# Kernel tuning notes

Hardware: AMD Instinct MI355X
Metric: run time of the kernel (lower is better)

The kernel has to match this reference:

```python
import jax, jax.numpy as jnp
import numpy as np

PATCH = 3
COMPLETENESS = 2.0


def setup_inputs() -> dict:
    key = jax.random.key(0)
    k1, k2, k3 = jax.random.split(key, 3)
    C, Hs, Ws, Hr, Wr = 64, 512, 512, 512, 512
    ref = jax.random.normal(k1, (C, Hr, Wr), dtype=jnp.float32)
    nnf_sr = jax.random.randint(k2, (Hs, Ws, 2), 0, 512, dtype=jnp.int32)  # (ry, rx) per src pixel
    nnf_rs = jax.random.randint(k3, (Hr, Wr, 2), 0, 512, dtype=jnp.int32)  # (sy, sx) per ref pixel
    return {"ref": ref, "nnf_sr": nnf_sr, "nnf_rs": nnf_rs}


def bds_vote(ref, nnf_sr, nnf_rs, patch=PATCH, completeness=COMPLETENESS):
    C, Hr, Wr = ref.shape
    Hs, Ws = nnf_sr.shape[0], nnf_sr.shape[1]
    h = patch // 2
    ws = 1.0 / (Hs * Ws)
    wr = completeness / (Hr * Wr)

    guide = jnp.zeros((C, Hs * Ws), dtype=ref.dtype)
    weight = jnp.zeros((Hs * Ws,), dtype=ref.dtype)

    def accumulate(guide, weight, sy, sx, ry, rx, w):
        # sy,sx: target (src) centers [N]; ry,rx: source (ref) centers [N]
        # Clipped patch extents of the original code are equivalent to per-pixel
        # validity: both target and ref offset coords must be in range.
        for dy in range(-h, h + 1):
            for dx in range(-h, h + 1):
                ty, tx = sy + dy, sx + dx
                qy, qx = ry + dy, rx + dx
                valid = ((ty >= 0) & (ty < Hs) & (tx >= 0) & (tx < Ws) &
                         (qy >= 0) & (qy < Hr) & (qx >= 0) & (qx < Wr))
                vmask = valid.astype(ref.dtype) * w
                idx = jnp.clip(ty, 0, Hs - 1) * Ws + jnp.clip(tx, 0, Ws - 1)
                vals = ref[:, jnp.clip(qy, 0, Hr - 1), jnp.clip(qx, 0, Wr - 1)] * vmask[None, :]
                guide = guide.at[:, idx].add(vals)
                weight = weight.at[idx].add(vmask)
        return guide, weight

    # source -> reference pass (weight ws)
    gy, gx = jnp.meshgrid(jnp.arange(Hs), jnp.arange(Ws), indexing='ij')
    guide, weight = accumulate(guide, weight,
                               gy.reshape(-1), gx.reshape(-1),
                               nnf_sr[..., 0].reshape(-1), nnf_sr[..., 1].reshape(-1), ws)
    # reference -> source pass (weight wr)
    ry, rx = jnp.meshgrid(jnp.arange(Hr), jnp.arange(Wr), indexing='ij')
    guide, weight = accumulate(guide, weight,
                               nnf_rs[..., 0].reshape(-1), nnf_rs[..., 1].reshape(-1),
                               ry.reshape(-1), rx.reshape(-1), wr)

    weight = jnp.where(weight == 0, jnp.asarray(1.0, ref.dtype), weight)
    return (guide / weight[None, :]).reshape(C, Hs, Ws)


def reference(ref, nnf_sr, nnf_rs):
    return bds_vote(ref, nnf_sr, nnf_rs)
```

## Files before the change

### kernel.cpp

```cpp
#include <hip/hip_runtime.h>

#define HS   512
#define WSZ  512
#define NC   64
#define HW   (HS * WSZ)
#define KCAP 16

typedef unsigned int uint;
typedef unsigned short ushort;

__device__ __forceinline__ ushort f2bf(float f) {
    uint b = __float_as_uint(f);
    return (ushort)((b + 0x7FFFu + ((b >> 16) & 1u)) >> 16);
}

__global__ __launch_bounds__(256) void prep_kernel(
    const float4* __restrict__ ref4, uint4* __restrict__ refu4,
    int* __restrict__ cnt)
{
    __shared__ float lds[64 * 65];
    const int p0  = blockIdx.x * 64;
    const int tid = threadIdx.x;
    if (tid < 64) cnt[blockIdx.x * 64 + tid] = 0;
#pragma unroll
    for (int k = 0; k < 4; ++k) {
        int e  = k * 256 + tid;
        int c  = e >> 4;
        int i4 = e & 15;
        float4 v = ref4[(size_t)c * (HW / 4) + (p0 >> 2) + i4];
        lds[(i4 * 4 + 0) * 65 + c] = v.x;
        lds[(i4 * 4 + 1) * 65 + c] = v.y;
        lds[(i4 * 4 + 2) * 65 + c] = v.z;
        lds[(i4 * 4 + 3) * 65 + c] = v.w;
    }
    __syncthreads();
#pragma unroll
    for (int k = 0; k < 2; ++k) {
        int e = k * 256 + tid;
        int i = e >> 3;
        int q = e & 7;
        const float* row = &lds[i * 65 + 8 * q];
        uint4 u;
        u.x = (uint)f2bf(row[0]) | ((uint)f2bf(row[1]) << 16);
        u.y = (uint)f2bf(row[2]) | ((uint)f2bf(row[3]) << 16);
        u.z = (uint)f2bf(row[4]) | ((uint)f2bf(row[5]) << 16);
        u.w = (uint)f2bf(row[6]) | ((uint)f2bf(row[7]) << 16);
        refu4[(size_t)(p0 + i) * 8 + q] = u;
    }
}

__global__ __launch_bounds__(256) void fill_bins(
    const int2* __restrict__ nnf_rs, int* __restrict__ cnt,
    int* __restrict__ slots)
{
    int r = blockIdx.x * 256 + threadIdx.x;
    int2 s = nnf_rs[r];
    int bin = (s.x << 9) | s.y;
    int pos = atomicAdd(&cnt[bin], 1);
    if (pos < KCAP) slots[(bin << 4) + pos] = r;
}

template <bool PACKED>
__global__ __launch_bounds__(256) void gather8(
    const uint4* __restrict__ refu4,
    const float* __restrict__ reff,
    const int2*  __restrict__ nnf_sr,
    const int*   __restrict__ cnt,
    const int*   __restrict__ slots,
    float* __restrict__ out)
{
    const float ws = 1.0f / 262144.0f;
    const float wr = 2.0f / 262144.0f;

    const int tid = threadIdx.x;
    const int k   = tid & 7;
    const int t   = blockIdx.x * 32 + (tid >> 3);
    const int ty  = t >> 9, tx = t & 511;

    float a0=0,a1=0,a2=0,a3=0,a4=0,a5=0,a6=0,a7=0, w=0.f;

#define ACCUM(qv, mv)                                                         \
    {                                                                         \
        const int   q_ = (qv);                                                \
        const float m_ = (mv);                                                \
        if (PACKED) {                                                         \
            uint4 u_ = refu4[(size_t)q_ * 8 + k];                             \
            a0 += __uint_as_float(u_.x << 16)         * m_;                   \
            a1 += __uint_as_float(u_.x & 0xffff0000u) * m_;                   \
            a2 += __uint_as_float(u_.y << 16)         * m_;                   \
            a3 += __uint_as_float(u_.y & 0xffff0000u) * m_;                   \
            a4 += __uint_as_float(u_.z << 16)         * m_;                   \
            a5 += __uint_as_float(u_.z & 0xffff0000u) * m_;                   \
            a6 += __uint_as_float(u_.w << 16)         * m_;                   \
            a7 += __uint_as_float(u_.w & 0xffff0000u) * m_;                   \
        } else {                                                              \
            const size_t c0_ = (size_t)(8 * k) * HW + q_;                     \
            a0 += reff[c0_ + 0*(size_t)HW] * m_;                              \
            a1 += reff[c0_ + 1*(size_t)HW] * m_;                              \
            a2 += reff[c0_ + 2*(size_t)HW] * m_;                              \
            a3 += reff[c0_ + 3*(size_t)HW] * m_;                              \
            a4 += reff[c0_ + 4*(size_t)HW] * m_;                              \
            a5 += reff[c0_ + 5*(size_t)HW] * m_;                              \
            a6 += reff[c0_ + 6*(size_t)HW] * m_;                              \
            a7 += reff[c0_ + 7*(size_t)HW] * m_;                              \
        }                                                                     \
        w += m_;                                                              \
    }

    int mt0,mt1,mt2,mt3,mt4,mt5,mt6,mt7,mt8;
    int run = 0;

#define TAP(i, dy, dx)                                                        \
    {                                                                         \
        const int sy = ty - (dy), sx = tx - (dx);                             \
        const bool sval = ((unsigned)sy < 512u) & ((unsigned)sx < 512u);      \
        const int sidx = ((sy & 511) << 9) | (sx & 511);                      \
        mt##i = (sidx << 12) | ((i) << 8) | run;                              \
        const int c = cnt[sidx];                                              \
        run += sval ? min(c, KCAP) : 0;                                       \
        const int2 nn = nnf_sr[sidx];                                         \
        const int qy = nn.x + (dy), qx = nn.y + (dx);                         \
        const bool v = sval & ((unsigned)qy < 512u) & ((unsigned)qx < 512u);  \
        ACCUM((((qy & 511) << 9) | (qx & 511)), v ? ws : 0.f)                 \
    }

    TAP(0, -1, -1)  TAP(1, -1, 0)  TAP(2, -1, 1)
    TAP(3,  0, -1)  TAP(4,  0, 0)  TAP(5,  0, 1)
    TAP(6,  1, -1)  TAP(7,  1, 0)  TAP(8,  1, 1)
#undef TAP

    const int S = run;

#define SEL(i)  m_ = (s_ >= (mt##i & 255)) ? mt##i : m_;
#define ENTRY(sv)                                                             \
    {                                                                         \
        const int s_ = (sv);                                                  \
        int m_ = mt0;                                                         \
        SEL(1) SEL(2) SEL(3) SEL(4) SEL(5) SEL(6) SEL(7) SEL(8)               \
        const int off_ = m_ & 255;                                            \
        const int ii_  = (m_ >> 8) & 15;                                      \
        const int bs_  = (m_ >> 12) << 4;           \
        const int idx_ = min(s_ - off_, KCAP - 1);                            \
        const int e_   = slots[bs_ + idx_];                                   \
        const int ry_  = (e_ >> 9) & 511, rx_ = e_ & 511;                     \
        const int dyp_ = (ii_ * 11) >> 5;                           \
        const int dy_  = dyp_ - 1, dx_ = ii_ - 3 * dyp_ - 1;                  \
        const int qy_  = ry_ + dy_, qx_ = rx_ + dx_;                          \
        const bool v_  = (s_ < S) &                                           \
                         ((unsigned)qy_ < 512u) & ((unsigned)qx_ < 512u);     \
        ACCUM((((qy_ & 511) << 9) | (qx_ & 511)), v_ ? wr : 0.f)              \
    }

    for (int s = 0; s < S; s += 2) {
        ENTRY(s)
        ENTRY(s + 1)
    }
#undef ENTRY
#undef SEL
#undef ACCUM

    if (w == 0.f) w = 1.f;
    const float inv = 1.f / w;
    size_t o = (size_t)(8 * k) * HW + t;
    out[o]                = a0 * inv;
    out[o + 1*(size_t)HW] = a1 * inv;
    out[o + 2*(size_t)HW] = a2 * inv;
    out[o + 3*(size_t)HW] = a3 * inv;
    out[o + 4*(size_t)HW] = a4 * inv;
    out[o + 5*(size_t)HW] = a5 * inv;
    out[o + 6*(size_t)HW] = a6 * inv;
    out[o + 7*(size_t)HW] = a7 * inv;
}

extern "C" void kernel_launch(void* const* d_in, const int* in_sizes, int n_in,
                              void* d_out, int out_size, void* d_ws, size_t ws_size,
                              hipStream_t stream)
{
    const float* ref    = (const float*)d_in[0];
    const int2*  nnf_sr = (const int2*)d_in[1];
    const int2*  nnf_rs = (const int2*)d_in[2];
    float* out = (float*)d_out;

    char* wsb = (char*)d_ws;
    const size_t refT_bytes = (size_t)HW * NC * 2;
    const size_t cnt_bytes  = (size_t)HW * 4;
    const size_t slot_bytes = (size_t)HW * KCAP * 4;

    if (ws_size >= refT_bytes + cnt_bytes + slot_bytes) {
        uint4* refu4 = (uint4*)wsb;
        int*   cntp  = (int*)(wsb + refT_bytes);
        int*   slots = (int*)(wsb + refT_bytes + cnt_bytes);

        prep_kernel<<<HW / 64, 256, 0, stream>>>((const float4*)ref, refu4, cntp);
        fill_bins<<<HW / 256, 256, 0, stream>>>(nnf_rs, cntp, slots);
        gather8<true><<<HW / 32, 256, 0, stream>>>(refu4, nullptr, nnf_sr,
                                                   cntp, slots, out);
    } else {
        int* cntp  = (int*)wsb;
        int* slots = cntp + HW;
        hipMemsetAsync(cntp, 0, cnt_bytes, stream);
        fill_bins<<<HW / 256, 256, 0, stream>>>(nnf_rs, cntp, slots);
        gather8<false><<<HW / 32, 256, 0, stream>>>(nullptr, ref, nnf_sr,
                                                    cntp, slots, out);
    }
}
```

Measured before the change: 236.5 us.

## Build per-block LDS lists of pre-validated ref contributions for completeness pass

Each block of 32 targets first gathers bin counts for a 3x34 neighborhood into LDS, then expands each source bin's slot entries into per-target lists of validated ref pixel indices, using LDS atomics. The gather phase then reads these compact lists with int4 loads instead of doing per-entry select chains, slot loads and bounds checks in every lane of the 8-lane group. This removes redundant slot reads (the old version repeated them across 8 channel lanes) and invalid-entry work, at the cost of two extra barriers, LDS atomics, and a hard cap of 32 entries per target that could drop contributions.

```diff
diff --git a/kernel.cpp b/kernel.cpp
--- a/kernel.cpp
+++ b/kernel.cpp
@@ -5,6 +5,7 @@
 #define NC   64
 #define HW   (HS * WSZ)
 #define KCAP 16
+#define LCAP 32
 
 typedef unsigned int uint;
 typedef unsigned short ushort;
@@ -60,10 +61,8 @@
     if (pos < KCAP) slots[(bin << 4) + pos] = r;
 }
 
-template <bool PACKED>
-__global__ __launch_bounds__(256) void gather8(
+__global__ __launch_bounds__(256) void gather_lds(
     const uint4* __restrict__ refu4,
-    const float* __restrict__ reff,
     const int2*  __restrict__ nnf_sr,
     const int*   __restrict__ cnt,
     const int*   __restrict__ slots,
@@ -72,10 +71,50 @@
     const float ws = 1.0f / 262144.0f;
     const float wr = 2.0f / 262144.0f;
 
+    __shared__ int lists[32][36];
+    __shared__ int lcnt[32];
+    __shared__ int bcnt[102];
+
     const int tid = threadIdx.x;
-    const int k   = tid & 7;
-    const int t   = blockIdx.x * 32 + (tid >> 3);
-    const int ty  = t >> 9, tx = t & 511;
+    const int t0  = blockIdx.x * 32;
+    const int ty0 = t0 >> 9, tx0 = t0 & 511;
+
+    if (tid < 32) lcnt[tid] = 0;
+    if (tid < 102) {
+        const int jr = tid / 34, jc = tid - jr * 34;
+        const int sy = ty0 + jr - 1, sx = tx0 + jc - 1;
+        const bool sv = ((unsigned)sy < 512u) & ((unsigned)sx < 512u);
+        bcnt[tid] = sv ? min(cnt[(sy << 9) | sx], KCAP) : 0;
+    }
+    __syncthreads();
+
+    for (int p = tid; p < 306; p += 256) {
+        const int j  = p / 3;
+        const int di = p - j * 3;
+        const int jr = j / 34, jc = j - jr * 34;
+        const int dy = 1 - jr;
+        const int dx = di - 1;
+        const int lt = jc - 1 + dx;
+        const int c  = bcnt[j];
+        if (((unsigned)lt < 32u) && (c > 0)) {
+            const int sy = ty0 + jr - 1, sx = tx0 + jc - 1;
+            const int sbase = (((sy << 9) | sx) << 4);
+            for (int e = 0; e < c; ++e) {
+                const int r  = slots[sbase + e];
+                const int qy = (r >> 9) + dy, qx = (r & 511) + dx;
+                if (((unsigned)qy < 512u) & ((unsigned)qx < 512u)) {
+                    const int pos = atomicAdd(&lcnt[lt], 1);
+                    if (pos < LCAP) lists[lt][pos] = (qy << 9) | qx;
+                }
+            }
+        }
+    }
+    __syncthreads();
+
+    const int k  = tid & 7;
+    const int lt = tid >> 3;
+    const int t  = t0 + lt;
+    const int ty = ty0, tx = t & 511;
 
     float a0=0,a1=0,a2=0,a3=0,a4=0,a5=0,a6=0,a7=0, w=0.f;
 
@@ -83,80 +122,42 @@
     {                                                                         \
         const int   q_ = (qv);                                                \
         const float m_ = (mv);                                                \
-        if (PACKED) {                                                         \
-            uint4 u_ = refu4[(size_t)q_ * 8 + k];                             \
-            a0 += __uint_as_float(u_.x << 16)         * m_;                   \
-            a1 += __uint_as_float(u_.x & 0xffff0000u) * m_;                   \
-            a2 += __uint_as_float(u_.y << 16)         * m_;                   \
-            a3 += __uint_as_float(u_.y & 0xffff0000u) * m_;                   \
-            a4 += __uint_as_float(u_.z << 16)         * m_;                   \
-            a5 += __uint_as_float(u_.z & 0xffff0000u) * m_;                   \
-            a6 += __uint_as_float(u_.w << 16)         * m_;                   \
-            a7 += __uint_as_float(u_.w & 0xffff0000u) * m_;                   \
-        } else {                                                              \
-            const size_t c0_ = (size_t)(8 * k) * HW + q_;                     \
-            a0 += reff[c0_ + 0*(size_t)HW] * m_;                              \
-            a1 += reff[c0_ + 1*(size_t)HW] * m_;                              \
-            a2 += reff[c0_ + 2*(size_t)HW] * m_;                              \
-            a3 += reff[c0_ + 3*(size_t)HW] * m_;                              \
-            a4 += reff[c0_ + 4*(size_t)HW] * m_;                              \
-            a5 += reff[c0_ + 5*(size_t)HW] * m_;                              \
-            a6 += reff[c0_ + 6*(size_t)HW] * m_;                              \
-            a7 += reff[c0_ + 7*(size_t)HW] * m_;                              \
-        }                                                                     \
+        uint4 u_ = refu4[(size_t)q_ * 8 + k];                                 \
+        a0 += __uint_as_float(u_.x << 16)         * m_;                       \
+        a1 += __uint_as_float(u_.x & 0xffff0000u) * m_;                       \
+        a2 += __uint_as_float(u_.y << 16)         * m_;                       \
+        a3 += __uint_as_float(u_.y & 0xffff0000u) * m_;                       \
+        a4 += __uint_as_float(u_.z << 16)         * m_;                       \
+        a5 += __uint_as_float(u_.z & 0xffff0000u) * m_;                       \
+        a6 += __uint_as_float(u_.w << 16)         * m_;                       \
+        a7 += __uint_as_float(u_.w & 0xffff0000u) * m_;                       \
         w += m_;                                                              \
     }
 
-    int mt0,mt1,mt2,mt3,mt4,mt5,mt6,mt7,mt8;
-    int run = 0;
-
-#define TAP(i, dy, dx)                                                        \
+#define TAP(dy, dx)                                                           \
     {                                                                         \
         const int sy = ty - (dy), sx = tx - (dx);                             \
         const bool sval = ((unsigned)sy < 512u) & ((unsigned)sx < 512u);      \
         const int sidx = ((sy & 511) << 9) | (sx & 511);                      \
-        mt##i = (sidx << 12) | ((i) << 8) | run;                              \
-        const int c = cnt[sidx];                                              \
-        run += sval ? min(c, KCAP) : 0;                                       \
         const int2 nn = nnf_sr[sidx];                                         \
         const int qy = nn.x + (dy), qx = nn.y + (dx);                         \
         const bool v = sval & ((unsigned)qy < 512u) & ((unsigned)qx < 512u);  \
         ACCUM((((qy & 511) << 9) | (qx & 511)), v ? ws : 0.f)                 \
     }
 
-    TAP(0, -1, -1)  TAP(1, -1, 0)  TAP(2, -1, 1)
-    TAP(3,  0, -1)  TAP(4,  0, 0)  TAP(5,  0, 1)
-    TAP(6,  1, -1)  TAP(7,  1, 0)  TAP(8,  1, 1)
+    TAP(-1, -1)  TAP(-1, 0)  TAP(-1, 1)
+    TAP( 0, -1)  TAP( 0, 0)  TAP( 0, 1)
+    TAP( 1, -1)  TAP( 1, 0)  TAP( 1, 1)
 #undef TAP
 
-    const int S = run;
-
-#define SEL(i)  m_ = (s_ >= (mt##i & 255)) ? mt##i : m_;
-#define ENTRY(sv)                                                             \
-    {                                                                         \
-        const int s_ = (sv);                                                  \
-        int m_ = mt0;                                                         \
-        SEL(1) SEL(2) SEL(3) SEL(4) SEL(5) SEL(6) SEL(7) SEL(8)               \
-        const int off_ = m_ & 255;                                            \
-        const int ii_  = (m_ >> 8) & 15;                                      \
-        const int bs_  = (m_ >> 12) << 4;           \
-        const int idx_ = min(s_ - off_, KCAP - 1);                            \
-        const int e_   = slots[bs_ + idx_];                                   \
-        const int ry_  = (e_ >> 9) & 511, rx_ = e_ & 511;                     \
-        const int dyp_ = (ii_ * 11) >> 5;                           \
-        const int dy_  = dyp_ - 1, dx_ = ii_ - 3 * dyp_ - 1;                  \
-        const int qy_  = ry_ + dy_, qx_ = rx_ + dx_;                          \
-        const bool v_  = (s_ < S) &                                           \
-                         ((unsigned)qy_ < 512u) & ((unsigned)qx_ < 512u);     \
-        ACCUM((((qy_ & 511) << 9) | (qx_ & 511)), v_ ? wr : 0.f)              \
-    }
-
-    for (int s = 0; s < S; s += 2) {
-        ENTRY(s)
-        ENTRY(s + 1)
-    }
-#undef ENTRY
-#undef SEL
+    const int S = min(lcnt[lt], LCAP);
+    for (int s = 0; s < S; s += 4) {
+        const int4 e4 = *(const int4*)&lists[lt][s];
+        ACCUM(e4.x & 0x3FFFF, wr)
+        ACCUM(e4.y & 0x3FFFF, (s + 1 < S) ? wr : 0.f)
+        ACCUM(e4.z & 0x3FFFF, (s + 2 < S) ? wr : 0.f)
+        ACCUM(e4.w & 0x3FFFF, (s + 3 < S) ? wr : 0.f)
+    }
 #undef ACCUM
 
     if (w == 0.f) w = 1.f;
@@ -172,6 +173,104 @@
     out[o + 7*(size_t)HW] = a7 * inv;
 }
 
+__global__ __launch_bounds__(256) void gather8_f32(
+    const float* __restrict__ reff,
+    const int2*  __restrict__ nnf_sr,
+    const int*   __restrict__ cnt,
+    const int*   __restrict__ slots,
+    float* __restrict__ out)
+{
+    const float ws = 1.0f / 262144.0f;
+    const float wr = 2.0f / 262144.0f;
+
+    const int tid = threadIdx.x;
+    const int k   = tid & 7;
+    const int t   = blockIdx.x * 32 + (tid >> 3);
+    const int ty  = t >> 9, tx = t & 511;
+
+    float a0=0,a1=0,a2=0,a3=0,a4=0,a5=0,a6=0,a7=0, w=0.f;
+
+#define ACCUM(qv, mv)                                                         \
+    {                                                                         \
+        const int   q_ = (qv);                                                \
+        const float m_ = (mv);                                                \
+        const size_t c0_ = (size_t)(8 * k) * HW + q_;                         \
+        a0 += reff[c0_ + 0*(size_t)HW] * m_;                                  \
+        a1 += reff[c0_ + 1*(size_t)HW] * m_;                                  \
+        a2 += reff[c0_ + 2*(size_t)HW] * m_;                                  \
+        a3 += reff[c0_ + 3*(size_t)HW] * m_;                                  \
+        a4 += reff[c0_ + 4*(size_t)HW] * m_;                                  \
+        a5 += reff[c0_ + 5*(size_t)HW] * m_;                                  \
+        a6 += reff[c0_ + 6*(size_t)HW] * m_;                                  \
+        a7 += reff[c0_ + 7*(size_t)HW] * m_;                                  \
+        w += m_;                                                              \
+    }
+
+    int mt0,mt1,mt2,mt3,mt4,mt5,mt6,mt7,mt8;
+    int run = 0;
+
+#define TAP(i, dy, dx)                                                        \
+    {                                                                         \
+        const int sy = ty - (dy), sx = tx - (dx);                             \
+        const bool sval = ((unsigned)sy < 512u) & ((unsigned)sx < 512u);      \
+        const int sidx = ((sy & 511) << 9) | (sx & 511);                      \
+        mt##i = (sidx << 12) | ((i) << 8) | run;                              \
+        const int c = cnt[sidx];                                              \
+        run += sval ? min(c, KCAP) : 0;                                       \
+        const int2 nn = nnf_sr[sidx];                                         \
+        const int qy = nn.x + (dy), qx = nn.y + (dx);                         \
+        const bool v = sval & ((unsigned)qy < 512u) & ((unsigned)qx < 512u);  \
+        ACCUM((((qy & 511) << 9) | (qx & 511)), v ? ws : 0.f)                 \
+    }
+
+    TAP(0, -1, -1)  TAP(1, -1, 0)  TAP(2, -1, 1)
+    TAP(3,  0, -1)  TAP(4,  0, 0)  TAP(5,  0, 1)
+    TAP(6,  1, -1)  TAP(7,  1, 0)  TAP(8,  1, 1)
+#undef TAP
+
+    const int S = run;
+
+#define SEL(i)  m_ = (s_ >= (mt##i & 255)) ? mt##i : m_;
+#define ENTRY(sv)                                                             \
+    {                                                                         \
+        const int s_ = (sv);                                                  \
+        int m_ = mt0;                                                         \
+        SEL(1) SEL(2) SEL(3) SEL(4) SEL(5) SEL(6) SEL(7) SEL(8)               \
+        const int off_ = m_ & 255;                                            \
+        const int ii_  = (m_ >> 8) & 15;                                      \
+        const int bs_  = (m_ >> 12) << 4;                                     \
+        const int idx_ = min(s_ - off_, KCAP - 1);                            \
+        const int e_   = slots[bs_ + idx_];                                   \
+        const int ry_  = (e_ >> 9) & 511, rx_ = e_ & 511;                     \
+        const int dyp_ = (ii_ * 11) >> 5;                                     \
+        const int dy_  = dyp_ - 1, dx_ = ii_ - 3 * dyp_ - 1;                  \
+        const int qy_  = ry_ + dy_, qx_ = rx_ + dx_;                          \
+        const bool v_  = (s_ < S) &                                           \
+                         ((unsigned)qy_ < 512u) & ((unsigned)qx_ < 512u);     \
+        ACCUM((((qy_ & 511) << 9) | (qx_ & 511)), v_ ? wr : 0.f)              \
+    }
+
+    for (int s = 0; s < S; s += 2) {
+        ENTRY(s)
+        ENTRY(s + 1)
+    }
+#undef ENTRY
+#undef SEL
+#undef ACCUM
+
+    if (w == 0.f) w = 1.f;
+    const float inv = 1.f / w;
+    size_t o = (size_t)(8 * k) * HW + t;
+    out[o]                = a0 * inv;
+    out[o + 1*(size_t)HW] = a1 * inv;
+    out[o + 2*(size_t)HW] = a2 * inv;
+    out[o + 3*(size_t)HW] = a3 * inv;
+    out[o + 4*(size_t)HW] = a4 * inv;
+    out[o + 5*(size_t)HW] = a5 * inv;
+    out[o + 6*(size_t)HW] = a6 * inv;
+    out[o + 7*(size_t)HW] = a7 * inv;
+}
+
 extern "C" void kernel_launch(void* const* d_in, const int* in_sizes, int n_in,
                               void* d_out, int out_size, void* d_ws, size_t ws_size,
                               hipStream_t stream)
@@ -193,14 +292,12 @@
 
         prep_kernel<<<HW / 64, 256, 0, stream>>>((const float4*)ref, refu4, cntp);
         fill_bins<<<HW / 256, 256, 0, stream>>>(nnf_rs, cntp, slots);
-        gather8<true><<<HW / 32, 256, 0, stream>>>(refu4, nullptr, nnf_sr,
-                                                   cntp, slots, out);
+        gather_lds<<<HW / 32, 256, 0, stream>>>(refu4, nnf_sr, cntp, slots, out);
     } else {
         int* cntp  = (int*)wsb;
         int* slots = cntp + HW;
         hipMemsetAsync(cntp, 0, cnt_bytes, stream);
         fill_bins<<<HW / 256, 256, 0, stream>>>(nnf_rs, cntp, slots);
-        gather8<false><<<HW / 32, 256, 0, stream>>>(nullptr, ref, nnf_sr,
-                                                    cntp, slots, out);
-    }
-}
+        gather8_f32<<<HW / 32, 256, 0, stream>>>(ref, nnf_sr, cntp, slots, out);
+    }
+}
```

New measurement: 227.4 us. -3.9%, faster.
